# Performance work log

Hardware: AMD Instinct MI355X
Metric: run time of the kernel (lower is better)

The kernel has to match this reference:

```python
import jax, jax.numpy as jnp
import numpy as np

N_HEADS = 4
HEAD_DIM = 64
N_EXPERTS = 64
TOP_K = 2
INPUT_DIM = 2048
N_TOKENS = 16384


def setup_inputs() -> dict:
    key = jax.random.key(0)
    ks = jax.random.split(key, 10)
    s = 0.02
    return {
        "x": jax.random.normal(ks[0], (N_TOKENS, INPUT_DIM), dtype=jnp.float32),
        "Wp": jax.random.normal(ks[1], (INPUT_DIM, N_HEADS * HEAD_DIM), dtype=jnp.float32) * s,
        "bp": jnp.zeros((N_HEADS * HEAD_DIM,), dtype=jnp.float32),
        "W1": jax.random.normal(ks[2], (N_HEADS, HEAD_DIM, HEAD_DIM), dtype=jnp.float32) * s,
        "b1": jnp.zeros((N_HEADS, HEAD_DIM), dtype=jnp.float32),
        "W2": jax.random.normal(ks[3], (N_HEADS, HEAD_DIM, N_EXPERTS), dtype=jnp.float32) * s,
        "b2": jnp.zeros((N_HEADS, N_EXPERTS), dtype=jnp.float32),
        "Wc": jax.random.normal(ks[4], (N_HEADS * N_EXPERTS, N_EXPERTS), dtype=jnp.float32) * s,
        "bc": jnp.zeros((N_EXPERTS,), dtype=jnp.float32),
        "temperature": jnp.ones((1,), dtype=jnp.float32) * 2.0,
        "noise_scale": jnp.ones((1,), dtype=jnp.float32) * 0.1,
    }


def reference(x, Wp, bp, W1, b1, W2, b2, Wc, bc, temperature, noise_scale):
    # eval-mode forward (no dropout, no routing noise)
    n = x.shape[0]
    h = (x @ Wp + bp).reshape(n, N_HEADS, HEAD_DIM)            # [N, 4, 64]
    hid = jax.nn.relu(jnp.einsum('nhd,hde->nhe', h, W1) + b1)   # [N, 4, 64]
    head_logits = jnp.einsum('nhd,hde->nhe', hid, W2) + b2      # [N, 4, E] (cat order = head order)
    combined = head_logits.reshape(n, N_HEADS * N_EXPERTS)      # [N, 4*E]
    gate_logits = combined @ Wc + bc                            # [N, E]
    gate_logits = gate_logits / jnp.clip(temperature, 0.5, 5.0)
    top_vals, top_idx = jax.lax.top_k(gate_logits, TOP_K)       # [N, k]
    top_gates = jax.nn.softmax(top_vals, axis=-1)
    gates = jnp.zeros_like(gate_logits).at[jnp.arange(n)[:, None], top_idx].set(top_gates)
    return gates, top_idx, gate_logits
```

## Files before the change

### kernel.cpp

```cpp
#include <hip/hip_runtime.h>
#include <math.h>

#define NT   16384
#define KD   2048
#define PROJ 256
#define NH   4
#define HD   64
#define NE   64

#define GATES_OFF 0
#define IDX_OFF   (NT * NE)
#define GL_OFF    (NT * NE + NT * 2)

typedef __attribute__((ext_vector_type(8))) short short8;
typedef __attribute__((ext_vector_type(4))) float f32x4;

static __device__ __forceinline__ ushort f2bf_rne(float f) {
    uint u = __float_as_uint(f);
    u += 0x7FFFu + ((u >> 16) & 1u);
    return (ushort)(u >> 16);
}
static __device__ __forceinline__ float bf2f(ushort b) {
    return __uint_as_float(((uint)b) << 16);
}

static __device__ __forceinline__ void gload16(const void* g, void* s) {
    __builtin_amdgcn_global_load_lds(
        (const __attribute__((address_space(1))) unsigned int*)g,
        (__attribute__((address_space(3))) unsigned int*)s, 16, 0, 0);
}

static __device__ __forceinline__ void split8(const float4 a, const float4 b,
                                              short8& hi8, short8& lo8)
{
    const float f[8] = { a.x, a.y, a.z, a.w, b.x, b.y, b.z, b.w };
    uint hp[4], lp[4];
#pragma unroll
    for (int i = 0; i < 4; ++i) {
        const uint u0 = __float_as_uint(f[2 * i]);
        const uint u1 = __float_as_uint(f[2 * i + 1]);
        hp[i] = (u0 >> 16) | (u1 & 0xFFFF0000u);
        const float r0 = f[2 * i]     - __uint_as_float(u0 & 0xFFFF0000u);
        const float r1 = f[2 * i + 1] - __uint_as_float(u1 & 0xFFFF0000u);
        lp[i] = (__float_as_uint(r0) >> 16) | (__float_as_uint(r1) & 0xFFFF0000u);
    }
    const uint4 hv = { hp[0], hp[1], hp[2], hp[3] };
    const uint4 lv = { lp[0], lp[1], lp[2], lp[3] };
    hi8 = *(const short8*)&hv;
    lo8 = *(const short8*)&lv;
}

__global__ __launch_bounds__(256) void k0_split(const float* __restrict__ Wp,
                                                ushort* __restrict__ WpT_hi,
                                                ushort* __restrict__ WpT_lo)
{
    __shared__ ushort Th[64][72];
    __shared__ ushort Tl[64][72];

    const int t  = threadIdx.x;
    const int kb = blockIdx.x * 64;
    const int cb = blockIdx.y * 64;

#pragma unroll
    for (int q = 0; q < 4; ++q) {
        const int s   = t + q * 256;
        const int row = s >> 4;
        const int c4  = (s & 15) * 4;
        const float4 v = *(const float4*)&Wp[(size_t)(kb + row) * PROJ + cb + c4];
        const float vv[4] = { v.x, v.y, v.z, v.w };
#pragma unroll
        for (int j = 0; j < 4; ++j) {
            const ushort hi = f2bf_rne(vv[j]);
            const ushort lo = f2bf_rne(vv[j] - bf2f(hi));
            Th[c4 + j][row] = hi;
            Tl[c4 + j][row] = lo;
        }
    }
    __syncthreads();

#pragma unroll
    for (int q = 0; q < 2; ++q) {
        const int s    = t + q * 256;
        const int crow = s >> 3;
        const int kq   = (s & 7) * 8;
        *(uint4*)&WpT_hi[(size_t)(cb + crow) * KD + kb + kq] = *(const uint4*)&Th[crow][kq];
        *(uint4*)&WpT_lo[(size_t)(cb + crow) * KD + kb + kq] = *(const uint4*)&Tl[crow][kq];
    }
}

__global__ __launch_bounds__(256, 2) void k1_mfma(const float* __restrict__ x,
                                                  const ushort* __restrict__ WpT_hi,
                                                  const ushort* __restrict__ WpT_lo,
                                                  const float* __restrict__ bp,
                                                  float* __restrict__ hT)
{
    __shared__ float  Abuf[2][4096];
    __shared__ ushort Bhbuf[2][2048];
    __shared__ ushort Blbuf[2][2048];

    const int t  = threadIdx.x;
    const int w  = t >> 6;
    const int l  = t & 63;
    const int wm = w >> 1;
    const int wn = w & 1;
    const int n0 = blockIdx.x * 64;
    const int m0 = blockIdx.y * 128;

    const float* asrc0;
    const float* asrc1;
    const float* asrc2;
    const float* asrc3;
    {
        const float* tmp[4];
#pragma unroll
        for (int j = 0; j < 4; ++j) {
            const int idx  = w * 4 + j;
            const int f    = idx >> 1;
            const int lf   = ((idx & 1) << 5) | (l >> 1);
            const int half = l & 1;
            const int row  = f * 16 + (lf & 15);
            const int kofs = (lf >> 4) * 8 + half * 4;
            tmp[j] = &x[(size_t)(m0 + row) * KD + kofs];
        }
        asrc0 = tmp[0]; asrc1 = tmp[1]; asrc2 = tmp[2]; asrc3 = tmp[3];
    }
    const ushort* bsrc_h = &WpT_hi[(size_t)(n0 + w * 16 + (l & 15)) * KD + (l >> 4) * 8];
    const ushort* bsrc_l = &WpT_lo[(size_t)(n0 + w * 16 + (l & 15)) * KD + (l >> 4) * 8];

    f32x4 acc[4][2];
#pragma unroll
    for (int m = 0; m < 4; ++m)
#pragma unroll
        for (int n = 0; n < 2; ++n) acc[m][n] = (f32x4){0.f, 0.f, 0.f, 0.f};

#define K1_STAGE(BUF, KB)                                                      \
    gload16(asrc0 + (KB), &Abuf[BUF][(w * 4 + 0) * 256]);                      \
    gload16(asrc1 + (KB), &Abuf[BUF][(w * 4 + 1) * 256]);                      \
    gload16(asrc2 + (KB), &Abuf[BUF][(w * 4 + 2) * 256]);                      \
    gload16(asrc3 + (KB), &Abuf[BUF][(w * 4 + 3) * 256]);                      \
    gload16(bsrc_h + (KB), &Bhbuf[BUF][w * 512]);                              \
    gload16(bsrc_l + (KB), &Blbuf[BUF][w * 512]);

#define K1_COMPUTE(BUF)                                                        \
    {                                                                          \
        short8 bh[2], bl[2];                                                   \
        _Pragma("unroll")                                                      \
        for (int n = 0; n < 2; ++n) {                                          \
            const int nf = wn * 2 + n;                                         \
            bh[n] = *(const short8*)&Bhbuf[BUF][(nf * 64 + l) * 8];            \
            bl[n] = *(const short8*)&Blbuf[BUF][(nf * 64 + l) * 8];            \
        }                                                                      \
        _Pragma("unroll")                                                      \
        for (int m = 0; m < 4; ++m) {                                          \
            const int mf = wm * 4 + m;                                         \
            const float4 a0 = *(const float4*)&Abuf[BUF][(mf * 64 + l) * 8];   \
            const float4 a1 = *(const float4*)&Abuf[BUF][(mf * 64 + l) * 8 + 4]; \
            short8 ah, al8;                                                    \
            split8(a0, a1, ah, al8);                                           \
            _Pragma("unroll")                                                  \
            for (int n = 0; n < 2; ++n) {                                      \
                acc[m][n] = __builtin_amdgcn_mfma_f32_16x16x32_bf16(ah, bh[n], acc[m][n], 0, 0, 0); \
                acc[m][n] = __builtin_amdgcn_mfma_f32_16x16x32_bf16(ah, bl[n], acc[m][n], 0, 0, 0); \
                acc[m][n] = __builtin_amdgcn_mfma_f32_16x16x32_bf16(al8, bh[n], acc[m][n], 0, 0, 0); \
            }                                                                  \
        }                                                                      \
    }

    K1_STAGE(0, 0);
    __syncthreads();

    for (int ti = 0; ti < KD / 32; ++ti) {
        const int buf = ti & 1;
        if (ti + 1 < KD / 32) { K1_STAGE(buf ^ 1, (ti + 1) * 32); }
        K1_COMPUTE(buf);
        __syncthreads();
    }

#pragma unroll
    for (int n = 0; n < 2; ++n) {
        const int col = n0 + (wn * 2 + n) * 16 + (l & 15);
        const float b = bp[col];
#pragma unroll
        for (int m = 0; m < 4; ++m) {
            const int tok = m0 + (wm * 4 + m) * 16 + (l >> 4) * 4;
            float4 st = { acc[m][n].x + b, acc[m][n].y + b,
                          acc[m][n].z + b, acc[m][n].w + b };
            *(float4*)&hT[(size_t)col * NT + tok] = st;
        }
    }
#undef K1_STAGE
#undef K1_COMPUTE
}

__global__ __launch_bounds__(256) void k2_heads(const float* __restrict__ hT,
                                                const float* __restrict__ W1,
                                                const float* __restrict__ b1,
                                                const float* __restrict__ W2,
                                                const float* __restrict__ b2,
                                                float* __restrict__ hlT)
{
    __shared__ float W1s[64][64];
    __shared__ float W2s[64][64];
    __shared__ float Hs[64][132];

    const int t    = threadIdx.x;
    const int eg   = t & 15;
    const int tg   = t >> 4;
    const int head = blockIdx.y;
    const int tok0 = blockIdx.x * 128;

    {
        const float4* g1 = (const float4*)(W1 + (size_t)head * HD * HD);
        const float4* g2 = (const float4*)(W2 + (size_t)head * HD * HD);
        float4* s1 = (float4*)&W1s[0][0];
        float4* s2 = (float4*)&W2s[0][0];
#pragma unroll
        for (int q = 0; q < 4; ++q) {
            s1[t + q * 256] = g1[t + q * 256];
            s2[t + q * 256] = g2[t + q * 256];
        }
    }
    const float4 b1v = *(const float4*)&b1[head * HD + eg * 4];
    const float4 b2v = *(const float4*)&b2[head * HD + eg * 4];
    __syncthreads();

    float acc[4][8];
    {
        const float bb[4] = { b1v.x, b1v.y, b1v.z, b1v.w };
#pragma unroll
        for (int j = 0; j < 4; ++j)
#pragma unroll
            for (int i = 0; i < 8; ++i) acc[j][i] = bb[j];
    }
    const float* hbase = &hT[(size_t)(head * HD) * NT + tok0 + tg * 8];
#pragma unroll 4
    for (int d = 0; d < HD; ++d) {
        const float4 w  = *(const float4*)&W1s[d][eg * 4];
        const float4 h0 = *(const float4*)&hbase[(size_t)d * NT];
        const float4 h1 = *(const float4*)&hbase[(size_t)d * NT + 4];
        const float wv[4] = { w.x, w.y, w.z, w.w };
        const float hv[8] = { h0.x, h0.y, h0.z, h0.w, h1.x, h1.y, h1.z, h1.w };
#pragma unroll
        for (int j = 0; j < 4; ++j)
#pragma unroll
            for (int i = 0; i < 8; ++i)
                acc[j][i] = fmaf(wv[j], hv[i], acc[j][i]);
    }
#pragma unroll
    for (int j = 0; j < 4; ++j) {
        float4 lo, hi;
        lo.x = fmaxf(acc[j][0], 0.f); lo.y = fmaxf(acc[j][1], 0.f);
        lo.z = fmaxf(acc[j][2], 0.f); lo.w = fmaxf(acc[j][3], 0.f);
        hi.x = fmaxf(acc[j][4], 0.f); hi.y = fmaxf(acc[j][5], 0.f);
        hi.z = fmaxf(acc[j][6], 0.f); hi.w = fmaxf(acc[j][7], 0.f);
        *(float4*)&Hs[eg * 4 + j][tg * 8]     = lo;
        *(float4*)&Hs[eg * 4 + j][tg * 8 + 4] = hi;
    }
    __syncthreads();

    {
        const float bb[4] = { b2v.x, b2v.y, b2v.z, b2v.w };
#pragma unroll
        for (int j = 0; j < 4; ++j)
#pragma unroll
            for (int i = 0; i < 8; ++i) acc[j][i] = bb[j];
    }
#pragma unroll 4
    for (int d = 0; d < HD; ++d) {
        const float4 w  = *(const float4*)&W2s[d][eg * 4];
        const float4 h0 = *(const float4*)&Hs[d][tg * 8];
        const float4 h1 = *(const float4*)&Hs[d][tg * 8 + 4];
        const float wv[4] = { w.x, w.y, w.z, w.w };
        const float hv[8] = { h0.x, h0.y, h0.z, h0.w, h1.x, h1.y, h1.z, h1.w };
#pragma unroll
        for (int j = 0; j < 4; ++j)
#pragma unroll
            for (int i = 0; i < 8; ++i)
                acc[j][i] = fmaf(wv[j], hv[i], acc[j][i]);
    }
#pragma unroll
    for (int j = 0; j < 4; ++j) {
        float4 lo = { acc[j][0], acc[j][1], acc[j][2], acc[j][3] };
        float4 hi = { acc[j][4], acc[j][5], acc[j][6], acc[j][7] };
        float* dst = &hlT[(size_t)(head * HD + eg * 4 + j) * NT + tok0 + tg * 8];
        *(float4*)&dst[0] = lo;
        *(float4*)&dst[4] = hi;
    }
}

__global__ __launch_bounds__(512) void k3_gate(const float* __restrict__ hlT,
                                               const float* __restrict__ Wc,
                                               const float* __restrict__ bc,
                                               const float* __restrict__ temp,
                                               float* __restrict__ out)
{
    const int t    = threadIdx.x;
    const int eg   = t & 15;
    const int tg   = t >> 4;
    const int tok0 = blockIdx.x * 64;

    const float tv  = fminf(fmaxf(temp[0], 0.5f), 5.0f);
    const float inv = 1.0f / tv;
    const float4 bcv = *(const float4*)&bc[eg * 4];

    float acc[4][2];
    acc[0][0] = bcv.x; acc[0][1] = bcv.x;
    acc[1][0] = bcv.y; acc[1][1] = bcv.y;
    acc[2][0] = bcv.z; acc[2][1] = bcv.z;
    acc[3][0] = bcv.w; acc[3][1] = bcv.w;

    const float* hb = &hlT[tok0 + tg * 2];
#pragma unroll 8
    for (int k = 0; k < PROJ; ++k) {
        const float2 hv = *(const float2*)&hb[(size_t)k * NT];
        const float4 wv = *(const float4*)&Wc[k * NE + eg * 4];
        const float wa[4] = { wv.x, wv.y, wv.z, wv.w };
#pragma unroll
        for (int j = 0; j < 4; ++j) {
            acc[j][0] = fmaf(wa[j], hv.x, acc[j][0]);
            acc[j][1] = fmaf(wa[j], hv.y, acc[j][1]);
        }
    }

#pragma unroll
    for (int i = 0; i < 2; ++i) {
        const int tok = tok0 + tg * 2 + i;
        float gl_[4];
#pragma unroll
        for (int j = 0; j < 4; ++j) gl_[j] = acc[j][i] * inv;

        float v1 = gl_[0]; int i1 = eg * 4;
#pragma unroll
        for (int j = 1; j < 4; ++j)
            if (gl_[j] > v1) { v1 = gl_[j]; i1 = eg * 4 + j; }
#pragma unroll
        for (int off = 8; off >= 1; off >>= 1) {
            const float ov = __shfl_xor(v1, off);
            const int   oi = __shfl_xor(i1, off);
            if (ov > v1 || (ov == v1 && oi < i1)) { v1 = ov; i1 = oi; }
        }
        float v2 = -INFINITY; int i2 = NE;
#pragma unroll
        for (int j = 0; j < 4; ++j) {
            const int e = eg * 4 + j;
            if (e != i1 && gl_[j] > v2) { v2 = gl_[j]; i2 = e; }
        }
#pragma unroll
        for (int off = 8; off >= 1; off >>= 1) {
            const float ov = __shfl_xor(v2, off);
            const int   oi = __shfl_xor(i2, off);
            if (ov > v2 || (ov == v2 && oi < i2)) { v2 = ov; i2 = oi; }
        }

        const float e2  = expf(v2 - v1);
        const float s   = 1.f + e2;
        const float g1v = 1.f / s;
        const float g2v = e2 / s;

        float4 gv;
        {
            const int e0 = eg * 4;
            gv.x = (e0 + 0 == i1) ? g1v : ((e0 + 0 == i2) ? g2v : 0.f);
            gv.y = (e0 + 1 == i1) ? g1v : ((e0 + 1 == i2) ? g2v : 0.f);
            gv.z = (e0 + 2 == i1) ? g1v : ((e0 + 2 == i2) ? g2v : 0.f);
            gv.w = (e0 + 3 == i1) ? g1v : ((e0 + 3 == i2) ? g2v : 0.f);
        }
        *(float4*)&out[GATES_OFF + (size_t)tok * NE + eg * 4] = gv;
        const float4 glv = { gl_[0], gl_[1], gl_[2], gl_[3] };
        *(float4*)&out[GL_OFF + (size_t)tok * NE + eg * 4] = glv;
        if (eg == 0) {
            out[IDX_OFF + (size_t)tok * 2 + 0] = (float)i1;
            out[IDX_OFF + (size_t)tok * 2 + 1] = (float)i2;
        }
    }
}

extern "C" void kernel_launch(void* const* d_in, const int* in_sizes, int n_in,
                              void* d_out, int out_size, void* d_ws, size_t ws_size,
                              hipStream_t stream)
{
    (void)in_sizes; (void)n_in; (void)out_size; (void)ws_size;

    const float* x    = (const float*)d_in[0];
    const float* Wp   = (const float*)d_in[1];
    const float* bp   = (const float*)d_in[2];
    const float* W1   = (const float*)d_in[3];
    const float* b1   = (const float*)d_in[4];
    const float* W2   = (const float*)d_in[5];
    const float* b2   = (const float*)d_in[6];
    const float* Wc   = (const float*)d_in[7];
    const float* bc   = (const float*)d_in[8];
    const float* temp = (const float*)d_in[9];

    float* out = (float*)d_out;
    float* hT  = (float*)d_ws;
    float* hlT = hT + (size_t)PROJ * NT;

    ushort* WpT_hi = (ushort*)hlT;
    ushort* WpT_lo = WpT_hi + (size_t)KD * PROJ;

    k0_split<<<dim3(KD / 64, PROJ / 64), 256, 0, stream>>>(Wp, WpT_hi, WpT_lo);
    k1_mfma <<<dim3(PROJ / 64, NT / 128), 256, 0, stream>>>(x, WpT_hi, WpT_lo, bp, hT);
    k2_heads<<<dim3(NT / 128, NH),        256, 0, stream>>>(hT, W1, b1, W2, b2, hlT);
    k3_gate <<<dim3(NT / 64),             512, 0, stream>>>(hlT, Wc, bc, temp, out);
}
```

Before: 244.6 us.

## Fold W2 into Wc, fuse head MLP with gate, swizzle k1 LDS layout

Adds a small precompute kernel that multiplies each head's W2 by its slice of Wc and folds b2 into the gate bias, so the second head matmul and the gate matmul become one 64x64 product per head. The head MLP and gate/top-k kernels are merged into one kernel that loops over heads and accumulates gate logits in registers, so the head-logit intermediate is never written to or read from global memory. The projection GEMM's global-to-LDS staging is also changed to an XOR-swizzled layout to reduce bank conflicts. The fused kernel has a quarter as many blocks as the old head kernel, and reassociating the products can shift rounding near top-k ties.

```diff
diff --git a/kernel.cpp b/kernel.cpp
--- a/kernel.cpp
+++ b/kernel.cpp
@@ -88,6 +88,71 @@
     }
 }
 
+__global__ __launch_bounds__(256) void k0c(const float* __restrict__ W2,
+                                           const float* __restrict__ Wc,
+                                           const float* __restrict__ b2,
+                                           float* __restrict__ W2c,
+                                           float* __restrict__ bcpart)
+{
+    __shared__ float W2sT[64][65];
+    __shared__ float Wcs[64][64];
+
+    const int t    = threadIdx.x;
+    const int head = blockIdx.x;
+
+    {
+        const float4* gc = (const float4*)(Wc + (size_t)head * 64 * NE);
+        float4* sc = (float4*)&Wcs[0][0];
+#pragma unroll
+        for (int q = 0; q < 4; ++q) sc[t + q * 256] = gc[t + q * 256];
+    }
+    {
+        const float* g2 = W2 + (size_t)head * HD * HD;
+#pragma unroll
+        for (int q = 0; q < 4; ++q) {
+            const int s = t + q * 256;
+            const int r = s >> 4;
+            const int c = (s & 15) * 4;
+            const float4 v = *(const float4*)&g2[r * HD + c];
+            W2sT[c + 0][r] = v.x; W2sT[c + 1][r] = v.y;
+            W2sT[c + 2][r] = v.z; W2sT[c + 3][r] = v.w;
+        }
+    }
+    __syncthreads();
+
+    const int eg = t & 15;
+    const int dg = t >> 4;
+    float acc[4][4];
+#pragma unroll
+    for (int i = 0; i < 4; ++i)
+#pragma unroll
+        for (int j = 0; j < 4; ++j) acc[i][j] = 0.f;
+
+    for (int d2 = 0; d2 < 64; ++d2) {
+        const float4 wc = *(const float4*)&Wcs[d2][eg * 4];
+        const float4 w2 = *(const float4*)&W2sT[d2][dg * 4];
+        const float wcv[4] = { wc.x, wc.y, wc.z, wc.w };
+        const float w2v[4] = { w2.x, w2.y, w2.z, w2.w };
+#pragma unroll
+        for (int i = 0; i < 4; ++i)
+#pragma unroll
+            for (int j = 0; j < 4; ++j)
+                acc[i][j] = fmaf(w2v[i], wcv[j], acc[i][j]);
+    }
+#pragma unroll
+    for (int i = 0; i < 4; ++i) {
+        float4 v = { acc[i][0], acc[i][1], acc[i][2], acc[i][3] };
+        *(float4*)&W2c[(size_t)head * 4096 + (dg * 4 + i) * 64 + eg * 4] = v;
+    }
+
+    if (t < 64) {
+        float p = 0.f;
+        for (int d = 0; d < 64; ++d)
+            p = fmaf(b2[head * HD + d], Wcs[d][t], p);
+        bcpart[head * NE + t] = p;
+    }
+}
+
 __global__ __launch_bounds__(256, 2) void k1_mfma(const float* __restrict__ x,
                                                   const ushort* __restrict__ WpT_hi,
                                                   const ushort* __restrict__ WpT_lo,
@@ -106,26 +171,22 @@
     const int n0 = blockIdx.x * 64;
     const int m0 = blockIdx.y * 128;
 
-    const float* asrc0;
-    const float* asrc1;
-    const float* asrc2;
-    const float* asrc3;
+    const float* asrc0; const float* asrc1;
+    const float* asrc2; const float* asrc3;
     {
         const float* tmp[4];
 #pragma unroll
-        for (int j = 0; j < 4; ++j) {
-            const int idx  = w * 4 + j;
-            const int f    = idx >> 1;
-            const int lf   = ((idx & 1) << 5) | (l >> 1);
-            const int half = l & 1;
-            const int row  = f * 16 + (lf & 15);
-            const int kofs = (lf >> 4) * 8 + half * 4;
-            tmp[j] = &x[(size_t)(m0 + row) * KD + kofs];
+        for (int p = 0; p < 4; ++p) {
+            const int row = p * 32 + (t >> 3);
+            const int kg  = (t & 7) ^ (row & 7);
+            tmp[p] = &x[(size_t)(m0 + row) * KD + kg * 4];
         }
         asrc0 = tmp[0]; asrc1 = tmp[1]; asrc2 = tmp[2]; asrc3 = tmp[3];
     }
-    const ushort* bsrc_h = &WpT_hi[(size_t)(n0 + w * 16 + (l & 15)) * KD + (l >> 4) * 8];
-    const ushort* bsrc_l = &WpT_lo[(size_t)(n0 + w * 16 + (l & 15)) * KD + (l >> 4) * 8];
+    const int bc_  = t >> 2;
+    const int bko  = (t & 3) ^ (bc_ & 3);
+    const ushort* bsrch = &WpT_hi[(size_t)(n0 + bc_) * KD + bko * 8];
+    const ushort* bsrcl = &WpT_lo[(size_t)(n0 + bc_) * KD + bko * 8];
 
     f32x4 acc[4][2];
 #pragma unroll
@@ -134,33 +195,36 @@
         for (int n = 0; n < 2; ++n) acc[m][n] = (f32x4){0.f, 0.f, 0.f, 0.f};
 
 #define K1_STAGE(BUF, KB)                                                      \
-    gload16(asrc0 + (KB), &Abuf[BUF][(w * 4 + 0) * 256]);                      \
-    gload16(asrc1 + (KB), &Abuf[BUF][(w * 4 + 1) * 256]);                      \
-    gload16(asrc2 + (KB), &Abuf[BUF][(w * 4 + 2) * 256]);                      \
-    gload16(asrc3 + (KB), &Abuf[BUF][(w * 4 + 3) * 256]);                      \
-    gload16(bsrc_h + (KB), &Bhbuf[BUF][w * 512]);                              \
-    gload16(bsrc_l + (KB), &Blbuf[BUF][w * 512]);
+    gload16(asrc0 + (KB), &Abuf[BUF][(0 * 256 + w * 64) * 4]);                 \
+    gload16(asrc1 + (KB), &Abuf[BUF][(1 * 256 + w * 64) * 4]);                 \
+    gload16(asrc2 + (KB), &Abuf[BUF][(2 * 256 + w * 64) * 4]);                 \
+    gload16(asrc3 + (KB), &Abuf[BUF][(3 * 256 + w * 64) * 4]);                 \
+    gload16(bsrch + (KB), &Bhbuf[BUF][w * 512]);                               \
+    gload16(bsrcl + (KB), &Blbuf[BUF][w * 512]);
 
 #define K1_COMPUTE(BUF)                                                        \
     {                                                                          \
         short8 bh[2], bl[2];                                                   \
         _Pragma("unroll")                                                      \
         for (int n = 0; n < 2; ++n) {                                          \
-            const int nf = wn * 2 + n;                                         \
-            bh[n] = *(const short8*)&Bhbuf[BUF][(nf * 64 + l) * 8];            \
-            bl[n] = *(const short8*)&Blbuf[BUF][(nf * 64 + l) * 8];            \
+            const int c  = (wn * 2 + n) * 16 + (l & 15);                       \
+            const int ph = c * 4 + ((l >> 4) ^ (c & 3));                       \
+            bh[n] = *(const short8*)&Bhbuf[BUF][ph * 8];                       \
+            bl[n] = *(const short8*)&Blbuf[BUF][ph * 8];                       \
         }                                                                      \
         _Pragma("unroll")                                                      \
         for (int m = 0; m < 4; ++m) {                                          \
-            const int mf = wm * 4 + m;                                         \
-            const float4 a0 = *(const float4*)&Abuf[BUF][(mf * 64 + l) * 8];   \
-            const float4 a1 = *(const float4*)&Abuf[BUF][(mf * 64 + l) * 8 + 4]; \
+            const int row = (wm * 4 + m) * 16 + (l & 15);                      \
+            const int p0  = row * 8 + (((l >> 4) * 2 + 0) ^ (row & 7));        \
+            const int p1  = row * 8 + (((l >> 4) * 2 + 1) ^ (row & 7));        \
+            const float4 a0 = *(const float4*)&Abuf[BUF][p0 * 4];              \
+            const float4 a1 = *(const float4*)&Abuf[BUF][p1 * 4];              \
             short8 ah, al8;                                                    \
             split8(a0, a1, ah, al8);                                           \
             _Pragma("unroll")                                                  \
             for (int n = 0; n < 2; ++n) {                                      \
-                acc[m][n] = __builtin_amdgcn_mfma_f32_16x16x32_bf16(ah, bh[n], acc[m][n], 0, 0, 0); \
-                acc[m][n] = __builtin_amdgcn_mfma_f32_16x16x32_bf16(ah, bl[n], acc[m][n], 0, 0, 0); \
+                acc[m][n] = __builtin_amdgcn_mfma_f32_16x16x32_bf16(ah,  bh[n], acc[m][n], 0, 0, 0); \
+                acc[m][n] = __builtin_amdgcn_mfma_f32_16x16x32_bf16(ah,  bl[n], acc[m][n], 0, 0, 0); \
                 acc[m][n] = __builtin_amdgcn_mfma_f32_16x16x32_bf16(al8, bh[n], acc[m][n], 0, 0, 0); \
             }                                                                  \
         }                                                                      \
@@ -192,142 +256,113 @@
 #undef K1_COMPUTE
 }
 
-__global__ __launch_bounds__(256) void k2_heads(const float* __restrict__ hT,
+__global__ __launch_bounds__(256) void k23_gate(const float* __restrict__ hT,
                                                 const float* __restrict__ W1,
                                                 const float* __restrict__ b1,
-                                                const float* __restrict__ W2,
-                                                const float* __restrict__ b2,
-                                                float* __restrict__ hlT)
+                                                const float* __restrict__ W2c,
+                                                const float* __restrict__ bcpart,
+                                                const float* __restrict__ bc,
+                                                const float* __restrict__ temp,
+                                                float* __restrict__ out)
 {
     __shared__ float W1s[64][64];
-    __shared__ float W2s[64][64];
+    __shared__ float W2cs[64][64];
     __shared__ float Hs[64][132];
 
     const int t    = threadIdx.x;
     const int eg   = t & 15;
     const int tg   = t >> 4;
-    const int head = blockIdx.y;
     const int tok0 = blockIdx.x * 128;
-
-    {
-        const float4* g1 = (const float4*)(W1 + (size_t)head * HD * HD);
-        const float4* g2 = (const float4*)(W2 + (size_t)head * HD * HD);
-        float4* s1 = (float4*)&W1s[0][0];
-        float4* s2 = (float4*)&W2s[0][0];
-#pragma unroll
-        for (int q = 0; q < 4; ++q) {
-            s1[t + q * 256] = g1[t + q * 256];
-            s2[t + q * 256] = g2[t + q * 256];
-        }
-    }
-    const float4 b1v = *(const float4*)&b1[head * HD + eg * 4];
-    const float4 b2v = *(const float4*)&b2[head * HD + eg * 4];
-    __syncthreads();
-
-    float acc[4][8];
-    {
-        const float bb[4] = { b1v.x, b1v.y, b1v.z, b1v.w };
-#pragma unroll
-        for (int j = 0; j < 4; ++j)
-#pragma unroll
-            for (int i = 0; i < 8; ++i) acc[j][i] = bb[j];
-    }
-    const float* hbase = &hT[(size_t)(head * HD) * NT + tok0 + tg * 8];
-#pragma unroll 4
-    for (int d = 0; d < HD; ++d) {
-        const float4 w  = *(const float4*)&W1s[d][eg * 4];
-        const float4 h0 = *(const float4*)&hbase[(size_t)d * NT];
-        const float4 h1 = *(const float4*)&hbase[(size_t)d * NT + 4];
-        const float wv[4] = { w.x, w.y, w.z, w.w };
-        const float hv[8] = { h0.x, h0.y, h0.z, h0.w, h1.x, h1.y, h1.z, h1.w };
-#pragma unroll
-        for (int j = 0; j < 4; ++j)
-#pragma unroll
-            for (int i = 0; i < 8; ++i)
-                acc[j][i] = fmaf(wv[j], hv[i], acc[j][i]);
-    }
-#pragma unroll
-    for (int j = 0; j < 4; ++j) {
-        float4 lo, hi;
-        lo.x = fmaxf(acc[j][0], 0.f); lo.y = fmaxf(acc[j][1], 0.f);
-        lo.z = fmaxf(acc[j][2], 0.f); lo.w = fmaxf(acc[j][3], 0.f);
-        hi.x = fmaxf(acc[j][4], 0.f); hi.y = fmaxf(acc[j][5], 0.f);
-        hi.z = fmaxf(acc[j][6], 0.f); hi.w = fmaxf(acc[j][7], 0.f);
-        *(float4*)&Hs[eg * 4 + j][tg * 8]     = lo;
-        *(float4*)&Hs[eg * 4 + j][tg * 8 + 4] = hi;
-    }
-    __syncthreads();
-
-    {
-        const float bb[4] = { b2v.x, b2v.y, b2v.z, b2v.w };
-#pragma unroll
-        for (int j = 0; j < 4; ++j)
-#pragma unroll
-            for (int i = 0; i < 8; ++i) acc[j][i] = bb[j];
-    }
-#pragma unroll 4
-    for (int d = 0; d < HD; ++d) {
-        const float4 w  = *(const float4*)&W2s[d][eg * 4];
-        const float4 h0 = *(const float4*)&Hs[d][tg * 8];
-        const float4 h1 = *(const float4*)&Hs[d][tg * 8 + 4];
-        const float wv[4] = { w.x, w.y, w.z, w.w };
-        const float hv[8] = { h0.x, h0.y, h0.z, h0.w, h1.x, h1.y, h1.z, h1.w };
-#pragma unroll
-        for (int j = 0; j < 4; ++j)
-#pragma unroll
-            for (int i = 0; i < 8; ++i)
-                acc[j][i] = fmaf(wv[j], hv[i], acc[j][i]);
-    }
-#pragma unroll
-    for (int j = 0; j < 4; ++j) {
-        float4 lo = { acc[j][0], acc[j][1], acc[j][2], acc[j][3] };
-        float4 hi = { acc[j][4], acc[j][5], acc[j][6], acc[j][7] };
-        float* dst = &hlT[(size_t)(head * HD + eg * 4 + j) * NT + tok0 + tg * 8];
-        *(float4*)&dst[0] = lo;
-        *(float4*)&dst[4] = hi;
-    }
-}
-
-__global__ __launch_bounds__(512) void k3_gate(const float* __restrict__ hlT,
-                                               const float* __restrict__ Wc,
-                                               const float* __restrict__ bc,
-                                               const float* __restrict__ temp,
-                                               float* __restrict__ out)
-{
-    const int t    = threadIdx.x;
-    const int eg   = t & 15;
-    const int tg   = t >> 4;
-    const int tok0 = blockIdx.x * 64;
 
     const float tv  = fminf(fmaxf(temp[0], 0.5f), 5.0f);
     const float inv = 1.0f / tv;
-    const float4 bcv = *(const float4*)&bc[eg * 4];
-
-    float acc[4][2];
-    acc[0][0] = bcv.x; acc[0][1] = bcv.x;
-    acc[1][0] = bcv.y; acc[1][1] = bcv.y;
-    acc[2][0] = bcv.z; acc[2][1] = bcv.z;
-    acc[3][0] = bcv.w; acc[3][1] = bcv.w;
-
-    const float* hb = &hlT[tok0 + tg * 2];
-#pragma unroll 8
-    for (int k = 0; k < PROJ; ++k) {
-        const float2 hv = *(const float2*)&hb[(size_t)k * NT];
-        const float4 wv = *(const float4*)&Wc[k * NE + eg * 4];
-        const float wa[4] = { wv.x, wv.y, wv.z, wv.w };
+
+    float accg[4][8];
+    {
+        float bcp[4];
 #pragma unroll
         for (int j = 0; j < 4; ++j) {
-            acc[j][0] = fmaf(wa[j], hv.x, acc[j][0]);
-            acc[j][1] = fmaf(wa[j], hv.y, acc[j][1]);
-        }
-    }
-
-#pragma unroll
-    for (int i = 0; i < 2; ++i) {
-        const int tok = tok0 + tg * 2 + i;
+            const int e = eg * 4 + j;
+            bcp[j] = bc[e] + bcpart[e] + bcpart[NE + e]
+                   + bcpart[2 * NE + e] + bcpart[3 * NE + e];
+        }
+#pragma unroll
+        for (int j = 0; j < 4; ++j)
+#pragma unroll
+            for (int i = 0; i < 8; ++i) accg[j][i] = bcp[j];
+    }
+
+    for (int head = 0; head < NH; ++head) {
+        __syncthreads();
+        {
+            const float4* g1 = (const float4*)(W1 + (size_t)head * HD * HD);
+            const float4* g2 = (const float4*)(W2c + (size_t)head * HD * HD);
+            float4* s1 = (float4*)&W1s[0][0];
+            float4* s2 = (float4*)&W2cs[0][0];
+#pragma unroll
+            for (int q = 0; q < 4; ++q) {
+                s1[t + q * 256] = g1[t + q * 256];
+                s2[t + q * 256] = g2[t + q * 256];
+            }
+        }
+        const float4 b1v = *(const float4*)&b1[head * HD + eg * 4];
+        __syncthreads();
+
+        float acc[4][8];
+        {
+            const float bb[4] = { b1v.x, b1v.y, b1v.z, b1v.w };
+#pragma unroll
+            for (int j = 0; j < 4; ++j)
+#pragma unroll
+                for (int i = 0; i < 8; ++i) acc[j][i] = bb[j];
+        }
+        const float* hbase = &hT[(size_t)(head * HD) * NT + tok0 + tg * 8];
+#pragma unroll 4
+        for (int d = 0; d < HD; ++d) {
+            const float4 w  = *(const float4*)&W1s[d][eg * 4];
+            const float4 h0 = *(const float4*)&hbase[(size_t)d * NT];
+            const float4 h1 = *(const float4*)&hbase[(size_t)d * NT + 4];
+            const float wv[4] = { w.x, w.y, w.z, w.w };
+            const float hv[8] = { h0.x, h0.y, h0.z, h0.w, h1.x, h1.y, h1.z, h1.w };
+#pragma unroll
+            for (int j = 0; j < 4; ++j)
+#pragma unroll
+                for (int i = 0; i < 8; ++i)
+                    acc[j][i] = fmaf(wv[j], hv[i], acc[j][i]);
+        }
+#pragma unroll
+        for (int j = 0; j < 4; ++j) {
+            float4 lo, hi;
+            lo.x = fmaxf(acc[j][0], 0.f); lo.y = fmaxf(acc[j][1], 0.f);
+            lo.z = fmaxf(acc[j][2], 0.f); lo.w = fmaxf(acc[j][3], 0.f);
+            hi.x = fmaxf(acc[j][4], 0.f); hi.y = fmaxf(acc[j][5], 0.f);
+            hi.z = fmaxf(acc[j][6], 0.f); hi.w = fmaxf(acc[j][7], 0.f);
+            *(float4*)&Hs[eg * 4 + j][tg * 8]     = lo;
+            *(float4*)&Hs[eg * 4 + j][tg * 8 + 4] = hi;
+        }
+        __syncthreads();
+
+#pragma unroll 4
+        for (int d = 0; d < HD; ++d) {
+            const float4 w  = *(const float4*)&W2cs[d][eg * 4];
+            const float4 h0 = *(const float4*)&Hs[d][tg * 8];
+            const float4 h1 = *(const float4*)&Hs[d][tg * 8 + 4];
+            const float wv[4] = { w.x, w.y, w.z, w.w };
+            const float hv[8] = { h0.x, h0.y, h0.z, h0.w, h1.x, h1.y, h1.z, h1.w };
+#pragma unroll
+            for (int j = 0; j < 4; ++j)
+#pragma unroll
+                for (int i = 0; i < 8; ++i)
+                    accg[j][i] = fmaf(wv[j], hv[i], accg[j][i]);
+        }
+    }
+
+#pragma unroll
+    for (int i = 0; i < 8; ++i) {
+        const int tok = tok0 + tg * 8 + i;
         float gl_[4];
 #pragma unroll
-        for (int j = 0; j < 4; ++j) gl_[j] = acc[j][i] * inv;
+        for (int j = 0; j < 4; ++j) gl_[j] = accg[j][i] * inv;
 
         float v1 = gl_[0]; int i1 = eg * 4;
 #pragma unroll
@@ -394,13 +429,13 @@
 
     float* out = (float*)d_out;
     float* hT  = (float*)d_ws;
-    float* hlT = hT + (size_t)PROJ * NT;
-
-    ushort* WpT_hi = (ushort*)hlT;
+    ushort* WpT_hi = (ushort*)(hT + (size_t)PROJ * NT);
     ushort* WpT_lo = WpT_hi + (size_t)KD * PROJ;
+    float*  W2c    = (float*)(WpT_lo + (size_t)KD * PROJ);
+    float*  bcpart = W2c + NH * HD * NE;
 
     k0_split<<<dim3(KD / 64, PROJ / 64), 256, 0, stream>>>(Wp, WpT_hi, WpT_lo);
+    k0c     <<<dim3(NH),                 256, 0, stream>>>(W2, Wc, b2, W2c, bcpart);
     k1_mfma <<<dim3(PROJ / 64, NT / 128), 256, 0, stream>>>(x, WpT_hi, WpT_lo, bp, hT);
-    k2_heads<<<dim3(NT / 128, NH),        256, 0, stream>>>(hT, W1, b1, W2, b2, hlT);
-    k3_gate <<<dim3(NT / 64),             512, 0, stream>>>(hlT, Wc, bc, temp, out);
-}
+    k23_gate<<<dim3(NT / 128),           256, 0, stream>>>(hT, W1, b1, W2c, bcpart, bc, temp, out);
+}
```

Result: faster. 209.7 us (median of 3 runs) (-14.3%).
